# Optimization experiments

Hardware: AMD Instinct MI355X
Metric: run time of the kernel (lower is better)

The kernel has to match this reference:

```python
import jax, jax.numpy as jnp
import numpy as np

B, C, Np, D = 16, 64, 128, 128
HT = 4      # time heads
HS = 4      # space heads (GAT)
F = D       # GAT out_channels
DK = D // 2 # q/k proj dim
TOPK = 8
NEG = -1e30

def ln(x, g, b):
    m = x.mean(-1, keepdims=True)
    v = jnp.mean((x - m) ** 2, axis=-1, keepdims=True)
    return (x - m) / jnp.sqrt(v + 1e-5) * g + b

def setup_inputs() -> dict:
    key = jax.random.key(0)
    ks = jax.random.split(key, 16)
    w = lambda k, s: (jax.random.normal(k, s, jnp.float32) * 0.02)
    return dict(
        H_in=jax.random.normal(ks[0], (B, C, Np, D), jnp.float32),
        static_adj=jax.random.normal(ks[1], (C, C), jnp.float32) * 0.1,
        attn_in_w=w(ks[2], (3 * D, D)), attn_in_b=jnp.zeros((3 * D,), jnp.float32),
        attn_out_w=w(ks[3], (D, D)), attn_out_b=jnp.zeros((D,), jnp.float32),
        ln1_g=jnp.ones((D,), jnp.float32), ln1_b=jnp.zeros((D,), jnp.float32),
        ln2_g=jnp.ones((D,), jnp.float32), ln2_b=jnp.zeros((D,), jnp.float32),
        ff1_w=w(ks[4], (4 * D, D)), ff1_b=jnp.zeros((4 * D,), jnp.float32),
        ff2_w=w(ks[5], (D, 4 * D)), ff2_b=jnp.zeros((D,), jnp.float32),
        tnorm_g=jnp.ones((D,), jnp.float32), tnorm_b=jnp.zeros((D,), jnp.float32),
        q_w=w(ks[6], (DK, D)), q_b=jnp.zeros((DK,), jnp.float32),
        k_w=w(ks[7], (DK, D)), k_b=jnp.zeros((DK,), jnp.float32),
        gat_w=w(ks[8], (HS, F, D)),
        gat_att_src=w(ks[9], (HS, F)), gat_att_dst=w(ks[10], (HS, F)),
        gat_bias=jnp.zeros((D,), jnp.float32),
        snorm_g=jnp.ones((D,), jnp.float32), snorm_b=jnp.zeros((D,), jnp.float32),
    )

def _forward(H_in, static_adj, attn_in_w, attn_in_b, attn_out_w, attn_out_b,
             ln1_g, ln1_b, ln2_g, ln2_b, ff1_w, ff1_b, ff2_w, ff2_b,
             tnorm_g, tnorm_b, q_w, q_b, k_w, k_b,
             gat_w, gat_att_src, gat_att_dst, gat_bias, snorm_g, snorm_b):
    dh = D // HT
    # ---- temporal transformer encoder layer (norm_first) on [B*C, Np, D]
    x0 = H_in.reshape(B * C, Np, D)
    h = ln(x0, ln1_g, ln1_b)
    qkv = h @ attn_in_w.T + attn_in_b
    q, k, v = jnp.split(qkv, 3, axis=-1)
    q = q.reshape(-1, Np, HT, dh).transpose(0, 2, 1, 3)
    k = k.reshape(-1, Np, HT, dh).transpose(0, 2, 1, 3)
    v = v.reshape(-1, Np, HT, dh).transpose(0, 2, 1, 3)
    att = jax.nn.softmax(jnp.einsum('nhqd,nhkd->nhqk', q, k) / jnp.sqrt(jnp.float32(dh)), axis=-1)
    o = jnp.einsum('nhqk,nhkd->nhqd', att, v).transpose(0, 2, 1, 3).reshape(-1, Np, D)
    x = x0 + (o @ attn_out_w.T + attn_out_b)
    h2 = ln(x, ln2_g, ln2_b)
    x = x + jax.nn.relu(h2 @ ff1_w.T + ff1_b) @ ff2_w.T + ff2_b
    H_temp = ln(x0 + x, tnorm_g, tnorm_b).reshape(B, C, Np, D)
    # ---- dynamic adjacency from temporal summary
    Hs = H_temp.mean(axis=2)                              # [B,C,D]
    q2 = Hs @ q_w.T + q_b
    k2 = Hs @ k_w.T + k_b
    sim = jnp.einsum('bcd,bed->bce', q2, k2) * (DK ** -0.5)
    A = jnp.tanh(sim) + static_adj[None]                  # [B,C,C]
    # ---- top-k edge mask per sample (row r -> its top-k cols, no self loops)
    kk = max(1, min(TOPK, C - 1))
    idx = jax.lax.top_k(A, kk)[1]                         # [B,C,kk]
    mask = jnp.any(jax.nn.one_hot(idx, C, dtype=bool), axis=2)  # [B,C,C]
    mask = mask & (~jnp.eye(C, dtype=bool)) & (A != 0)
    # ---- dense masked GAT over all (B, Np) graphs; src=row, dst=col
    xh = jnp.einsum('bcpd,hfd->bphcf', H_temp, gat_w)     # [B,Np,HS,C,F]
    asrc = jnp.einsum('bphcf,hf->bphc', xh, gat_att_src)
    adst = jnp.einsum('bphcf,hf->bphc', xh, gat_att_dst)
    e = asrc[..., :, None] + adst[..., None, :]           # [B,Np,HS,src,dst]
    e = jnp.where(e > 0, e, 0.2 * e)                      # LeakyReLU(0.2)
    mb = mask[:, None, None, :, :]
    e = jnp.where(mb, e, NEG)
    e = e - e.max(axis=3, keepdims=True)                  # softmax over src per dst
    wgt = jnp.exp(e) * mb
    s = wgt.sum(axis=3, keepdims=True)
    a = wgt / jnp.where(s > 0, s, 1.0)
    out = jnp.einsum('bphst,bphsf->bphtf', a, xh).mean(axis=2) + gat_bias  # [B,Np,C,F]
    out = out.transpose(0, 2, 1, 3)                       # [B,C,Np,D]
    return ln(out + H_temp, snorm_g, snorm_b)

def reference(H_in, static_adj, attn_in_w, attn_in_b, attn_out_w, attn_out_b,
              ln1_g, ln1_b, ln2_g, ln2_b, ff1_w, ff1_b, ff2_w, ff2_b,
              tnorm_g, tnorm_b, q_w, q_b, k_w, k_b,
              gat_w, gat_att_src, gat_att_dst, gat_bias, snorm_g, snorm_b):
    return _forward(H_in, static_adj, attn_in_w, attn_in_b, attn_out_w, attn_out_b,
                    ln1_g, ln1_b, ln2_g, ln2_b, ff1_w, ff1_b, ff2_w, ff2_b,
                    tnorm_g, tnorm_b, q_w, q_b, k_w, k_b,
                    gat_w, gat_att_src, gat_att_dst, gat_bias, snorm_g, snorm_b)
```

## Files before the change

kernel.cpp:

```cpp
#include <hip/hip_runtime.h>
#include <cstdint>


typedef __attribute__((ext_vector_type(8)))  short bf16x8;
typedef __attribute__((ext_vector_type(16))) float f32x16;
#define MFMA32(a, b, c) __builtin_amdgcn_mfma_f32_32x32x16_bf16((a), (b), (c), 0, 0, 0)

__device__ __forceinline__ unsigned short f2bf(float f) {
    unsigned int u = __float_as_uint(f);
    u += 0x7fffu + ((u >> 16) & 1u);
    return (unsigned short)(u >> 16);
}
__device__ __forceinline__ float bf2f(unsigned short u) {
    return __uint_as_float(((unsigned int)u) << 16);
}

__device__ __forceinline__ bf16x8 lds_frag(const unsigned short* p) {
    union { bf16x8 v; ushort4 h[2]; } u;
    u.h[0] = *(const ushort4*)p;
    u.h[1] = *(const ushort4*)(p + 4);
    return u.v;
}
__device__ __forceinline__ bf16x8 gfrag(const unsigned short* p) {
    union { bf16x8 v; uint4 u; } t;
    t.u = *(const uint4*)p;
    return t.v;
}

__device__ __forceinline__ int rowmap(int r, int hl) { return (r & 3) + 8 * (r >> 2) + 4 * hl; }

__global__ void wconv_kernel(const float* __restrict__ wqkv, const float* __restrict__ wout,
                             const float* __restrict__ w1, const float* __restrict__ w2,
                             const float* __restrict__ gw,
                             unsigned short* __restrict__ dst) {
    int i = blockIdx.x * 256 + threadIdx.x;
    float v;
    if (i < 49152)       v = wqkv[i];
    else if (i < 65536)  v = wout[i - 49152];
    else if (i < 131072) v = w1[i - 65536];
    else if (i < 196608) v = w2[i - 131072];
    else                 v = gw[i - 196608];
    dst[i] = f2bf(v);
}

__global__ void wa_kernel(const float* __restrict__ gw, const float* __restrict__ asw,
                          const float* __restrict__ adw,
                          float* __restrict__ waS, float* __restrict__ waD) {
    int t = blockIdx.x * 256 + threadIdx.x;
    int h = t >> 8, d = (t >> 1) & 127, which = t & 1;
    const float* av = which ? adw : asw;
    float s = 0.f;
    for (int f = 0; f < 128; f++) s += av[h * 128 + f] * gw[(h * 128 + f) * 128 + d];
    (which ? waD : waS)[h * 128 + d] = s;
}

__global__ __launch_bounds__(256, 2)
void temporal_kernel(const float* __restrict__ Hin,
                     const unsigned short* __restrict__ wqkv_b, const float* __restrict__ bqkv,
                     const unsigned short* __restrict__ wout_b, const float* __restrict__ bout,
                     const float* __restrict__ g1, const float* __restrict__ b1,
                     const float* __restrict__ g2, const float* __restrict__ b2,
                     const unsigned short* __restrict__ w1_b, const float* __restrict__ bf1,
                     const unsigned short* __restrict__ w2_b, const float* __restrict__ bf2,
                     const float* __restrict__ tg, const float* __restrict__ tb,
                     float* __restrict__ Htemp) {
    __shared__ unsigned short RA[128][132];
    __shared__ double RBd[4512];
    unsigned short (*qb)[36]  = (unsigned short(*)[36])RBd;
    unsigned short (*kb)[36]  = (unsigned short(*)[36])((char*)RBd + 9216);
    unsigned short (*vT)[132] = (unsigned short(*)[132])((char*)RBd + 18432);
    unsigned short (*Pb)[36]  = (unsigned short(*)[36])((char*)RBd + 26880);
    unsigned short (*h2b)[132] = (unsigned short(*)[132])RBd;

    const int n = blockIdx.x;
    const int tid = threadIdx.x;
    const int lane = tid & 63;
    const int wv = tid >> 6;
    const int hl = lane >> 5;
    const int l31 = lane & 31;
    const int myrow = wv * 32 + l31;

    {
        int row = tid >> 1, hf = tid & 1;
        const float* src = Hin + ((long)n * 128 + row) * 128 + hf * 64;
        float xv[64];
        float s = 0.f, qs = 0.f;
#pragma unroll
        for (int i = 0; i < 64; i += 4) {
            float4 t = *(const float4*)(src + i);
            xv[i] = t.x; xv[i+1] = t.y; xv[i+2] = t.z; xv[i+3] = t.w;
        }
#pragma unroll
        for (int i = 0; i < 64; i++) { s += xv[i]; qs += xv[i] * xv[i]; }
        s += __shfl_xor(s, 1); qs += __shfl_xor(qs, 1);
        float mu = s * 0.0078125f;
        float rs = rsqrtf(fmaxf(qs * 0.0078125f - mu * mu, 0.f) + 1e-5f);
#pragma unroll
        for (int i = 0; i < 64; i++) {
            int d = hf * 64 + i;
            RA[row][d] = f2bf((xv[i] - mu) * rs * g1[d] + b1[d]);
        }
    }

    f32x16 oaccH[4];
#pragma unroll
    for (int h = 0; h < 4; h++)
#pragma unroll
        for (int r = 0; r < 16; r++) oaccH[h][r] = 0.f;

    for (int h = 0; h < 4; h++) {
        {
            f32x16 accq, acck, accv;
            float bq = bqkv[      h * 32 + l31];
            float bk = bqkv[128 + h * 32 + l31];
            float bv = bqkv[256 + h * 32 + l31];
#pragma unroll
            for (int r = 0; r < 16; r++) { accq[r] = bq; acck[r] = bk; accv[r] = bv; }
            const unsigned short* wq = wqkv_b + (      h * 32 + l31) * 128 + hl * 8;
            const unsigned short* wk = wqkv_b + (128 + h * 32 + l31) * 128 + hl * 8;
            const unsigned short* wvp= wqkv_b + (256 + h * 32 + l31) * 128 + hl * 8;
#pragma unroll
            for (int k0 = 0; k0 < 128; k0 += 16) {
                bf16x8 a  = lds_frag(&RA[myrow][k0 + hl * 8]);
                accq = MFMA32(a, gfrag(wq + k0), accq);
                acck = MFMA32(a, gfrag(wk + k0), acck);
                accv = MFMA32(a, gfrag(wvp + k0), accv);
            }
#pragma unroll
            for (int r = 0; r < 16; r++) {
                int tok = wv * 32 + rowmap(r, hl);
                qb[tok][l31] = f2bf(accq[r]);
                kb[tok][l31] = f2bf(acck[r]);
                vT[l31][tok] = f2bf(accv[r]);
            }
        }
        __syncthreads();

        f32x16 sacc[4];
#pragma unroll
        for (int t = 0; t < 4; t++)
#pragma unroll
            for (int r = 0; r < 16; r++) sacc[t][r] = 0.f;
#pragma unroll
        for (int k0 = 0; k0 < 32; k0 += 16) {
            bf16x8 a = lds_frag(&qb[myrow][k0 + hl * 8]);
#pragma unroll
            for (int t = 0; t < 4; t++) {
                bf16x8 b = lds_frag(&kb[t * 32 + l31][k0 + hl * 8]);
                sacc[t] = MFMA32(a, b, sacc[t]);
            }
        }
        const float scale = 0.17677669529663687f;
#pragma unroll
        for (int r = 0; r < 16; r++) {
            float m0 = fmaxf(fmaxf(sacc[0][r], sacc[1][r]), fmaxf(sacc[2][r], sacc[3][r]));
#pragma unroll
            for (int d = 1; d < 32; d <<= 1) m0 = fmaxf(m0, __shfl_xor(m0, d));
            float ssum = 0.f;
#pragma unroll
            for (int t = 0; t < 4; t++) {
                float e = __expf(scale * (sacc[t][r] - m0));
                sacc[t][r] = e; ssum += e;
            }
#pragma unroll
            for (int d = 1; d < 32; d <<= 1) ssum += __shfl_xor(ssum, d);
            float rinv = 1.f / ssum;
#pragma unroll
            for (int t = 0; t < 4; t++) sacc[t][r] *= rinv;
        }

#pragma unroll
        for (int t = 0; t < 4; t++) {
#pragma unroll
            for (int r = 0; r < 16; r++)
                Pb[wv * 32 + rowmap(r, hl)][l31] = f2bf(sacc[t][r]);
#pragma unroll
            for (int k0 = 0; k0 < 32; k0 += 16) {
                bf16x8 a = lds_frag(&Pb[wv * 32 + l31][k0 + hl * 8]);
                bf16x8 b = lds_frag(&vT[l31][t * 32 + k0 + hl * 8]);
                oaccH[h] = MFMA32(a, b, oaccH[h]);
            }
        }
        __syncthreads();
    }

#pragma unroll
    for (int h = 0; h < 4; h++)
#pragma unroll
        for (int r = 0; r < 16; r++) {
            int tok = wv * 32 + rowmap(r, hl);
            RA[tok][h * 32 + l31] = f2bf(oaccH[h][r]);
        }

    f32x16 acc[4];
#pragma unroll
    for (int t = 0; t < 4; t++) {
        float bo = bout[t * 32 + l31];
#pragma unroll
        for (int r = 0; r < 16; r++) {
            int tok = wv * 32 + rowmap(r, hl);
            acc[t][r] = Hin[((long)n * 128 + tok) * 128 + t * 32 + l31] + bo;
        }
    }
#pragma unroll
    for (int k0 = 0; k0 < 128; k0 += 16) {
        bf16x8 a = lds_frag(&RA[myrow][k0 + hl * 8]);
#pragma unroll
        for (int t = 0; t < 4; t++) {
            bf16x8 b = gfrag(wout_b + (t * 32 + l31) * 128 + k0 + hl * 8);
            acc[t] = MFMA32(a, b, acc[t]);
        }
    }

#pragma unroll
    for (int r = 0; r < 16; r++) {
        float s = acc[0][r] + acc[1][r] + acc[2][r] + acc[3][r];
#pragma unroll
        for (int d = 1; d < 32; d <<= 1) s += __shfl_xor(s, d);
        float mu = s * 0.0078125f;
        float q = 0.f;
#pragma unroll
        for (int t = 0; t < 4; t++) { float dv = acc[t][r] - mu; q += dv * dv; }
#pragma unroll
        for (int d = 1; d < 32; d <<= 1) q += __shfl_xor(q, d);
        float rs = rsqrtf(q * 0.0078125f + 1e-5f);
        int row = wv * 32 + rowmap(r, hl);
#pragma unroll
        for (int t = 0; t < 4; t++) {
            int col = t * 32 + l31;
            h2b[row][col] = f2bf((acc[t][r] - mu) * rs * g2[col] + b2[col]);
        }
    }

    f32x16 acc2[4];
#pragma unroll
    for (int t = 0; t < 4; t++) {
        float bv = bf2[t * 32 + l31];
#pragma unroll
        for (int r = 0; r < 16; r++) acc2[t][r] = acc[t][r] + bv;
    }

    for (int j = 0; j < 4; j++) {
        f32x16 racc[4];
#pragma unroll
        for (int t = 0; t < 4; t++) {
            float bv = bf1[j * 128 + t * 32 + l31];
#pragma unroll
            for (int r = 0; r < 16; r++) racc[t][r] = bv;
        }
#pragma unroll
        for (int k0 = 0; k0 < 128; k0 += 16) {
            bf16x8 a = lds_frag(&h2b[myrow][k0 + hl * 8]);
#pragma unroll
            for (int t = 0; t < 4; t++) {
                bf16x8 b = gfrag(w1_b + (j * 128 + t * 32 + l31) * 128 + k0 + hl * 8);
                racc[t] = MFMA32(a, b, racc[t]);
            }
        }
#pragma unroll
        for (int t = 0; t < 4; t++)
#pragma unroll
            for (int r = 0; r < 16; r++) {
                int row = wv * 32 + rowmap(r, hl);
                RA[row][t * 32 + l31] = f2bf(fmaxf(racc[t][r], 0.f));
            }
#pragma unroll
        for (int k0 = 0; k0 < 128; k0 += 16) {
            bf16x8 a = lds_frag(&RA[myrow][k0 + hl * 8]);
#pragma unroll
            for (int t = 0; t < 4; t++) {
                bf16x8 b = gfrag(w2_b + (t * 32 + l31) * 512 + j * 128 + k0 + hl * 8);
                acc2[t] = MFMA32(a, b, acc2[t]);
            }
        }
    }

#pragma unroll
    for (int t = 0; t < 4; t++)
#pragma unroll
        for (int r = 0; r < 16; r++) {
            int tok = wv * 32 + rowmap(r, hl);
            acc2[t][r] += Hin[((long)n * 128 + tok) * 128 + t * 32 + l31];
        }
    float* outf = Htemp + (long)n * 16384;
#pragma unroll
    for (int r = 0; r < 16; r++) {
        float s = acc2[0][r] + acc2[1][r] + acc2[2][r] + acc2[3][r];
#pragma unroll
        for (int d = 1; d < 32; d <<= 1) s += __shfl_xor(s, d);
        float mu = s * 0.0078125f;
        float q = 0.f;
#pragma unroll
        for (int t = 0; t < 4; t++) { float dv = acc2[t][r] - mu; q += dv * dv; }
#pragma unroll
        for (int d = 1; d < 32; d <<= 1) q += __shfl_xor(q, d);
        float rs = rsqrtf(q * 0.0078125f + 1e-5f);
        int tok = wv * 32 + rowmap(r, hl);
#pragma unroll
        for (int t = 0; t < 4; t++) {
            int col = t * 32 + l31;
            outf[tok * 128 + col] = (acc2[t][r] - mu) * rs * tg[col] + tb[col];
        }
    }
}

__global__ void hs_kernel(const float* __restrict__ Htemp, float* __restrict__ Hs) {
    int idx = blockIdx.x * 256 + threadIdx.x;
    int n = idx >> 7, d = idx & 127;
    float s = 0.f;
    for (int p = 0; p < 128; p++) s += Htemp[((long)n * 128 + p) * 128 + d];
    Hs[idx] = s * 0.0078125f;
}

__global__ __launch_bounds__(256)
void graph_kernel(const float* __restrict__ Hs,
                  const float* __restrict__ qw, const float* __restrict__ qb,
                  const float* __restrict__ kw, const float* __restrict__ kb,
                  const float* __restrict__ adj, unsigned long long* __restrict__ masks) {
    __shared__ float q2l[64][65];
    __shared__ float k2l[64][65];
    __shared__ float am[64][65];
    int b = blockIdx.x;
    int tid = threadIdx.x;
    {
        int r = tid & 127, jh = tid >> 7;
        int row = r & 63;
        const float* wmat = (r < 64) ? qw : kw;
        const float* bvec = (r < 64) ? qb : kb;
        const float* src = Hs + (long)(b * 64 + row) * 128;
        for (int jj = 0; jj < 32; jj++) {
            int j = jh * 32 + jj;
            const float* wrow = wmat + (long)j * 128;
            float s0 = 0.f, s1 = 0.f, s2 = 0.f, s3 = 0.f;
#pragma unroll
            for (int d = 0; d < 128; d += 4) {
                s0 += src[d] * wrow[d];     s1 += src[d+1] * wrow[d+1];
                s2 += src[d+2] * wrow[d+2]; s3 += src[d+3] * wrow[d+3];
            }
            float val = ((s0 + s1) + (s2 + s3)) + bvec[j];
            if (r < 64) q2l[row][j] = val; else k2l[row][j] = val;
        }
    }
    __syncthreads();
    {
        int c = tid & 63, eq = tid >> 6;
        for (int ee = 0; ee < 16; ee++) {
            int e = eq * 16 + ee;
            float s0 = 0.f, s1 = 0.f, s2 = 0.f, s3 = 0.f;
#pragma unroll
            for (int j = 0; j < 64; j += 4) {
                s0 += q2l[c][j]   * k2l[e][j];
                s1 += q2l[c][j+1] * k2l[e][j+1];
                s2 += q2l[c][j+2] * k2l[e][j+2];
                s3 += q2l[c][j+3] * k2l[e][j+3];
            }
            float sim = ((s0 + s1) + (s2 + s3)) * 0.125f;
            am[c][e] = tanhf(sim) + adj[c * 64 + e];
        }
    }
    __syncthreads();
    if (tid < 64) {
        int c = tid;
        unsigned long long sel = 0ull;
        for (int it = 0; it < 8; it++) {
            float best = -1e38f; int bi = 0;
            for (int e = 0; e < 64; e++) {
                float v = am[c][e];
                bool ok = (((sel >> e) & 1ull) == 0ull) && (v > best);
                best = ok ? v : best;
                bi = ok ? e : bi;
            }
            sel |= (1ull << bi);
        }
        sel &= ~(1ull << c);
        for (int e = 0; e < 64; e++)
            if (am[c][e] == 0.f) sel &= ~(1ull << e);
        masks[b * 64 + c] = sel;
    }
}

__global__ __launch_bounds__(256, 1)
void gat_kernel(float* __restrict__ Htemp,
                const unsigned short* __restrict__ gwb,
                const float* __restrict__ waS, const float* __restrict__ waD,
                const float* __restrict__ gbias,
                const unsigned long long* __restrict__ masks,
                const float* __restrict__ sg, const float* __restrict__ sb) {
    __shared__ unsigned short Htb[64][132];
    __shared__ double ovl_d[3264];
    __shared__ float asrcF[4][64], adstF[4][64];
    __shared__ float pmax[4][64], psum[4][64];
    __shared__ unsigned long long mk[64];

    unsigned short (*xhT)[68]  = (unsigned short(*)[68])ovl_d;
    unsigned short (*attT)[68] = (unsigned short(*)[68])((char*)ovl_d + 17408);
    float (*part)[8][64]       = (float(*)[8][64])ovl_d;

    const int bp = blockIdx.x;
    const int b = bp >> 7, p = bp & 127;
    const int tid = threadIdx.x;
    const int lane = tid & 63, wv = tid >> 6;
    const int hl = lane >> 5, l31 = lane & 31;
    const int rs = (wv & 1) * 32;
    const int cs = (wv >> 1) * 64;

    {
        int c = tid >> 2, qq = tid & 3;
        const float* src = Htemp + ((long)(b * 64 + c) * 128 + p) * 128 + qq * 32;
#pragma unroll
        for (int k = 0; k < 8; k++) {
            float4 t4 = *(const float4*)(src + 4 * k);
            ushort4 u; u.x = f2bf(t4.x); u.y = f2bf(t4.y); u.z = f2bf(t4.z); u.w = f2bf(t4.w);
            *(ushort4*)&Htb[c][qq * 32 + 4 * k] = u;
        }
    }
    if (tid < 64) mk[tid] = masks[b * 64 + tid];
    __syncthreads();

    {
        int s = lane, q = wv;
        float acc[8];
#pragma unroll
        for (int m = 0; m < 8; m++) acc[m] = 0.f;
        const unsigned int* hp = (const unsigned int*)&Htb[s][q * 32];
#pragma unroll
        for (int d2 = 0; d2 < 16; d2++) {
            unsigned int u = hp[d2];
            float f0 = __uint_as_float(u << 16);
            float f1 = __uint_as_float(u & 0xffff0000u);
            int d = q * 32 + 2 * d2;
#pragma unroll
            for (int h = 0; h < 4; h++) {
                acc[2*h]   += f0 * waS[h * 128 + d] + f1 * waS[h * 128 + d + 1];
                acc[2*h+1] += f0 * waD[h * 128 + d] + f1 * waD[h * 128 + d + 1];
            }
        }
#pragma unroll
        for (int m = 0; m < 8; m++) part[q][m][s] = acc[m];
    }
    __syncthreads();
    for (int o = tid; o < 512; o += 256) {
        int h = o >> 7, rem = o & 127, which = rem >> 6, s = rem & 63;
        int m = h * 2 + which;
        float v = part[0][m][s] + part[1][m][s] + part[2][m][s] + part[3][m][s];
        if (which == 0) asrcF[h][s] = v; else adstF[h][s] = v;
    }
    __syncthreads();

    f32x16 oacc0, oacc1;
#pragma unroll
    for (int r = 0; r < 16; r++) { oacc0[r] = 0.f; oacc1[r] = 0.f; }

    for (int h = 0; h < 4; h++) {
        f32x16 a0, a1;
#pragma unroll
        for (int r = 0; r < 16; r++) { a0[r] = 0.f; a1[r] = 0.f; }
        const unsigned short* gwh = gwb + h * 16384;
#pragma unroll
        for (int k0 = 0; k0 < 128; k0 += 16) {
            bf16x8 af = lds_frag(&Htb[rs + l31][k0 + hl * 8]);
            bf16x8 b0 = gfrag(gwh + (cs + l31) * 128 + k0 + hl * 8);
            bf16x8 b1 = gfrag(gwh + (cs + 32 + l31) * 128 + k0 + hl * 8);
            a0 = MFMA32(af, b0, a0);
            a1 = MFMA32(af, b1, a1);
        }
#pragma unroll
        for (int g = 0; g < 4; g++) {
            ushort4 u0, u1;
            u0.x = f2bf(a0[4*g]);   u0.y = f2bf(a0[4*g+1]);
            u0.z = f2bf(a0[4*g+2]); u0.w = f2bf(a0[4*g+3]);
            u1.x = f2bf(a1[4*g]);   u1.y = f2bf(a1[4*g+1]);
            u1.z = f2bf(a1[4*g+2]); u1.w = f2bf(a1[4*g+3]);
            int so = rs + 4 * hl + 8 * g;
            *(ushort4*)&xhT[cs + l31][so]      = u0;
            *(ushort4*)&xhT[cs + 32 + l31][so] = u1;
        }
        __syncthreads();

        {
            int t = lane;
            float adv = adstF[h][t];
            float ev[16];
            float mx = -1e30f;
#pragma unroll
            for (int i = 0; i < 16; i++) {
                int s = wv * 16 + i;
                float e = asrcF[h][s] + adv;
                e = (e > 0.f) ? e : 0.2f * e;
                ev[i] = e;
                if ((mk[s] >> t) & 1ull) mx = fmaxf(mx, e);
            }
            pmax[wv][t] = mx;
            __syncthreads();
            float M = fmaxf(fmaxf(pmax[0][t], pmax[1][t]), fmaxf(pmax[2][t], pmax[3][t]));
            float sm = 0.f;
#pragma unroll
            for (int i = 0; i < 16; i++) {
                int s = wv * 16 + i;
                float w = ((mk[s] >> t) & 1ull) ? __expf(ev[i] - M) : 0.f;
                ev[i] = w; sm += w;
            }
            psum[wv][t] = sm;
            __syncthreads();
            float S = psum[0][t] + psum[1][t] + psum[2][t] + psum[3][t];
            float rinv = (S > 0.f) ? 1.f / S : 0.f;
#pragma unroll
            for (int g = 0; g < 4; g++) {
                ushort4 u;
                u.x = f2bf(ev[4*g]   * rinv); u.y = f2bf(ev[4*g+1] * rinv);
                u.z = f2bf(ev[4*g+2] * rinv); u.w = f2bf(ev[4*g+3] * rinv);
                *(ushort4*)&attT[t][wv * 16 + 4 * g] = u;
            }
        }
        __syncthreads();

#pragma unroll
        for (int k0 = 0; k0 < 64; k0 += 16) {
            bf16x8 af = lds_frag(&attT[rs + l31][k0 + hl * 8]);
            bf16x8 b0 = lds_frag(&xhT[cs + l31][k0 + hl * 8]);
            bf16x8 b1 = lds_frag(&xhT[cs + 32 + l31][k0 + hl * 8]);
            oacc0 = MFMA32(af, b0, oacc0);
            oacc1 = MFMA32(af, b1, oacc1);
        }
        __syncthreads();
    }

    float gb0 = gbias[cs + l31], gb1 = gbias[cs + 32 + l31];
    float v0[16], v1[16];
#pragma unroll
    for (int r = 0; r < 16; r++) {
        int c = rs + rowmap(r, hl);
        v0[r] = oacc0[r] * 0.25f + gb0 + bf2f(Htb[c][cs + l31]);
        v1[r] = oacc1[r] * 0.25f + gb1 + bf2f(Htb[c][cs + 32 + l31]);
    }
#pragma unroll
    for (int r = 0; r < 16; r++) {
        float s = v0[r] + v1[r];
        float q = v0[r] * v0[r] + v1[r] * v1[r];
#pragma unroll
        for (int d = 1; d < 32; d <<= 1) { s += __shfl_xor(s, d); q += __shfl_xor(q, d); }
        if (l31 == 0) {
            int c = rs + rowmap(r, hl);
            pmax[wv >> 1][c] = s;
            psum[wv >> 1][c] = q;
        }
    }
    __syncthreads();
    float sgv0 = sg[cs + l31], sbv0 = sb[cs + l31];
    float sgv1 = sg[cs + 32 + l31], sbv1 = sb[cs + 32 + l31];
#pragma unroll
    for (int r = 0; r < 16; r++) {
        int c = rs + rowmap(r, hl);
        float sum = pmax[0][c] + pmax[1][c];
        float sq  = psum[0][c] + psum[1][c];
        float mu = sum * 0.0078125f;
        float var = sq * 0.0078125f - mu * mu;
        float rsd = rsqrtf(fmaxf(var, 0.f) + 1e-5f);
        float* orow = Htemp + ((long)(b * 64 + c) * 128 + p) * 128;
        orow[cs + l31]      = (v0[r] - mu) * rsd * sgv0 + sbv0;
        orow[cs + 32 + l31] = (v1[r] - mu) * rsd * sgv1 + sbv1;
    }
}

extern "C" void kernel_launch(void* const* d_in, const int* in_sizes, int n_in,
                              void* d_out, int out_size, void* d_ws, size_t ws_size,
                              hipStream_t stream) {
    const float* Hin        = (const float*)d_in[0];
    const float* static_adj = (const float*)d_in[1];
    const float* attn_in_w  = (const float*)d_in[2];
    const float* attn_in_b  = (const float*)d_in[3];
    const float* attn_out_w = (const float*)d_in[4];
    const float* attn_out_b = (const float*)d_in[5];
    const float* ln1_g      = (const float*)d_in[6];
    const float* ln1_b      = (const float*)d_in[7];
    const float* ln2_g      = (const float*)d_in[8];
    const float* ln2_b      = (const float*)d_in[9];
    const float* ff1_w      = (const float*)d_in[10];
    const float* ff1_b      = (const float*)d_in[11];
    const float* ff2_w      = (const float*)d_in[12];
    const float* ff2_b      = (const float*)d_in[13];
    const float* tnorm_g    = (const float*)d_in[14];
    const float* tnorm_b    = (const float*)d_in[15];
    const float* q_w        = (const float*)d_in[16];
    const float* q_b        = (const float*)d_in[17];
    const float* k_w        = (const float*)d_in[18];
    const float* k_b        = (const float*)d_in[19];
    const float* gat_w      = (const float*)d_in[20];
    const float* gat_att_src= (const float*)d_in[21];
    const float* gat_att_dst= (const float*)d_in[22];
    const float* gat_bias   = (const float*)d_in[23];
    const float* snorm_g    = (const float*)d_in[24];
    const float* snorm_b    = (const float*)d_in[25];

    float* out = (float*)d_out;
    char* ws = (char*)d_ws;
    unsigned short* wb = (unsigned short*)ws;
    const unsigned short* wqkv_b = wb;
    const unsigned short* wout_b = wb + 49152;
    const unsigned short* w1_b   = wb + 65536;
    const unsigned short* w2_b   = wb + 131072;
    const unsigned short* gw_b   = wb + 196608;
    unsigned long long* masks = (unsigned long long*)(ws + 524288);
    float* Hs  = (float*)(ws + 532480);
    float* waS = (float*)(ws + 1056768);
    float* waD = (float*)(ws + 1058816);

    hipLaunchKernelGGL(wconv_kernel, dim3(1024), dim3(256), 0, stream,
                       attn_in_w, attn_out_w, ff1_w, ff2_w, gat_w, wb);
    hipLaunchKernelGGL(wa_kernel, dim3(4), dim3(256), 0, stream,
                       gat_w, gat_att_src, gat_att_dst, waS, waD);
    hipLaunchKernelGGL(temporal_kernel, dim3(1024), dim3(256), 0, stream,
                       Hin, wqkv_b, attn_in_b, wout_b, attn_out_b,
                       ln1_g, ln1_b, ln2_g, ln2_b,
                       w1_b, ff1_b, w2_b, ff2_b, tnorm_g, tnorm_b, out);
    hipLaunchKernelGGL(hs_kernel, dim3(512), dim3(256), 0, stream, out, Hs);
    hipLaunchKernelGGL(graph_kernel, dim3(16), dim3(256), 0, stream,
                       Hs, q_w, q_b, k_w, k_b, static_adj, masks);
    hipLaunchKernelGGL(gat_kernel, dim3(2048), dim3(256), 0, stream,
                       out, gw_b, waS, waD, gat_bias,
                       masks, snorm_g, snorm_b);
}
```

Measured before the change: 621.9 us.

## Keep Q and P in registers via permlane swaps and shrink LDS for occupancy

The temporal kernel now computes Q transposed (weights as the A operand) and packs the accumulator directly into MFMA B-fragments with v_permlane32_swap. This drops the qb LDS buffer. The softmax probabilities are repacked the same way instead of going through the Pb LDS buffer, and with the transposed layout the row reductions need only one cross-lane shuffle instead of five. The FFN hidden activations go through a small per-wave scratch and layernorm output reuses RA, so LDS shrinks and launch bounds rise to 3 blocks per CU. The risk is register pressure at the higher occupancy target, which could cause spills.

```diff
diff --git a/kernel.cpp b/kernel.cpp
--- a/kernel.cpp
+++ b/kernel.cpp
@@ -28,6 +28,23 @@
 }
 
 __device__ __forceinline__ int rowmap(int r, int hl) { return (r & 3) + 8 * (r >> 2) + 4 * hl; }
+
+__device__ __forceinline__ unsigned int pk2(float lo, float hi) {
+    return (unsigned int)f2bf(lo) | ((unsigned int)f2bf(hi) << 16);
+}
+
+template<int B>
+__device__ __forceinline__ bf16x8 pack_frag(const f32x16& p) {
+    unsigned int a0 = pk2(p[B + 0], p[B + 1]);
+    unsigned int a1 = pk2(p[B + 2], p[B + 3]);
+    unsigned int b0 = pk2(p[B + 4], p[B + 5]);
+    unsigned int b1 = pk2(p[B + 6], p[B + 7]);
+    asm("v_permlane32_swap_b32 %0, %1" : "+v"(b0), "+v"(a0));
+    asm("v_permlane32_swap_b32 %0, %1" : "+v"(b1), "+v"(a1));
+    union { bf16x8 v; unsigned int w[4]; } u;
+    u.w[0] = a0; u.w[1] = a1; u.w[2] = b0; u.w[3] = b1;
+    return u.v;
+}
 
 __global__ void wconv_kernel(const float* __restrict__ wqkv, const float* __restrict__ wout,
                              const float* __restrict__ w1, const float* __restrict__ w2,
@@ -54,7 +71,7 @@
     (which ? waD : waS)[h * 128 + d] = s;
 }
 
-__global__ __launch_bounds__(256, 2)
+__global__ __launch_bounds__(256, 3)
 void temporal_kernel(const float* __restrict__ Hin,
                      const unsigned short* __restrict__ wqkv_b, const float* __restrict__ bqkv,
                      const unsigned short* __restrict__ wout_b, const float* __restrict__ bout,
@@ -65,12 +82,10 @@
                      const float* __restrict__ tg, const float* __restrict__ tb,
                      float* __restrict__ Htemp) {
     __shared__ unsigned short RA[128][132];
-    __shared__ double RBd[4512];
-    unsigned short (*qb)[36]  = (unsigned short(*)[36])RBd;
-    unsigned short (*kb)[36]  = (unsigned short(*)[36])((char*)RBd + 9216);
-    unsigned short (*vT)[132] = (unsigned short(*)[132])((char*)RBd + 18432);
-    unsigned short (*Pb)[36]  = (unsigned short(*)[36])((char*)RBd + 26880);
-    unsigned short (*h2b)[132] = (unsigned short(*)[132])RBd;
+    __shared__ double RBd[2208];
+    unsigned short (*kb)[36]  = (unsigned short(*)[36])RBd;
+    unsigned short (*vT)[132] = (unsigned short(*)[132])((char*)RBd + 9216);
+    unsigned short (*rscr)[32][36] = (unsigned short(*)[32][36])RBd;
 
     const int n = blockIdx.x;
     const int tid = threadIdx.x;
@@ -109,30 +124,33 @@
         for (int r = 0; r < 16; r++) oaccH[h][r] = 0.f;
 
     for (int h = 0; h < 4; h++) {
+        bf16x8 qf0, qf1;
         {
             f32x16 accq, acck, accv;
-            float bq = bqkv[      h * 32 + l31];
+#pragma unroll
+            for (int r = 0; r < 16; r++) accq[r] = bqkv[h * 32 + rowmap(r, hl)];
             float bk = bqkv[128 + h * 32 + l31];
             float bv = bqkv[256 + h * 32 + l31];
 #pragma unroll
-            for (int r = 0; r < 16; r++) { accq[r] = bq; acck[r] = bk; accv[r] = bv; }
+            for (int r = 0; r < 16; r++) { acck[r] = bk; accv[r] = bv; }
             const unsigned short* wq = wqkv_b + (      h * 32 + l31) * 128 + hl * 8;
             const unsigned short* wk = wqkv_b + (128 + h * 32 + l31) * 128 + hl * 8;
             const unsigned short* wvp= wqkv_b + (256 + h * 32 + l31) * 128 + hl * 8;
 #pragma unroll
             for (int k0 = 0; k0 < 128; k0 += 16) {
                 bf16x8 a  = lds_frag(&RA[myrow][k0 + hl * 8]);
-                accq = MFMA32(a, gfrag(wq + k0), accq);
+                accq = MFMA32(gfrag(wq + k0), a, accq);
                 acck = MFMA32(a, gfrag(wk + k0), acck);
                 accv = MFMA32(a, gfrag(wvp + k0), accv);
             }
 #pragma unroll
             for (int r = 0; r < 16; r++) {
                 int tok = wv * 32 + rowmap(r, hl);
-                qb[tok][l31] = f2bf(accq[r]);
                 kb[tok][l31] = f2bf(acck[r]);
                 vT[l31][tok] = f2bf(accv[r]);
             }
+            qf0 = pack_frag<0>(accq);
+            qf1 = pack_frag<8>(accq);
         }
         __syncthreads();
 
@@ -142,44 +160,42 @@
 #pragma unroll
             for (int r = 0; r < 16; r++) sacc[t][r] = 0.f;
 #pragma unroll
-        for (int k0 = 0; k0 < 32; k0 += 16) {
-            bf16x8 a = lds_frag(&qb[myrow][k0 + hl * 8]);
-#pragma unroll
-            for (int t = 0; t < 4; t++) {
-                bf16x8 b = lds_frag(&kb[t * 32 + l31][k0 + hl * 8]);
-                sacc[t] = MFMA32(a, b, sacc[t]);
-            }
+        for (int t = 0; t < 4; t++) {
+            bf16x8 ka0 = lds_frag(&kb[t * 32 + l31][hl * 8]);
+            sacc[t] = MFMA32(ka0, qf0, sacc[t]);
+            bf16x8 ka1 = lds_frag(&kb[t * 32 + l31][16 + hl * 8]);
+            sacc[t] = MFMA32(ka1, qf1, sacc[t]);
         }
         const float scale = 0.17677669529663687f;
-#pragma unroll
-        for (int r = 0; r < 16; r++) {
-            float m0 = fmaxf(fmaxf(sacc[0][r], sacc[1][r]), fmaxf(sacc[2][r], sacc[3][r]));
-#pragma unroll
-            for (int d = 1; d < 32; d <<= 1) m0 = fmaxf(m0, __shfl_xor(m0, d));
-            float ssum = 0.f;
-#pragma unroll
-            for (int t = 0; t < 4; t++) {
+        float m0 = -1e30f;
+#pragma unroll
+        for (int t = 0; t < 4; t++)
+#pragma unroll
+            for (int r = 0; r < 16; r++) m0 = fmaxf(m0, sacc[t][r]);
+        m0 = fmaxf(m0, __shfl_xor(m0, 32));
+        float ssum = 0.f;
+#pragma unroll
+        for (int t = 0; t < 4; t++)
+#pragma unroll
+            for (int r = 0; r < 16; r++) {
                 float e = __expf(scale * (sacc[t][r] - m0));
                 sacc[t][r] = e; ssum += e;
             }
-#pragma unroll
-            for (int d = 1; d < 32; d <<= 1) ssum += __shfl_xor(ssum, d);
-            float rinv = 1.f / ssum;
-#pragma unroll
-            for (int t = 0; t < 4; t++) sacc[t][r] *= rinv;
-        }
+        ssum += __shfl_xor(ssum, 32);
+        float rinv = 1.f / ssum;
+#pragma unroll
+        for (int t = 0; t < 4; t++)
+#pragma unroll
+            for (int r = 0; r < 16; r++) sacc[t][r] *= rinv;
 
 #pragma unroll
         for (int t = 0; t < 4; t++) {
-#pragma unroll
-            for (int r = 0; r < 16; r++)
-                Pb[wv * 32 + rowmap(r, hl)][l31] = f2bf(sacc[t][r]);
-#pragma unroll
-            for (int k0 = 0; k0 < 32; k0 += 16) {
-                bf16x8 a = lds_frag(&Pb[wv * 32 + l31][k0 + hl * 8]);
-                bf16x8 b = lds_frag(&vT[l31][t * 32 + k0 + hl * 8]);
-                oaccH[h] = MFMA32(a, b, oaccH[h]);
-            }
+            bf16x8 pf0 = pack_frag<0>(sacc[t]);
+            bf16x8 v0  = lds_frag(&vT[l31][t * 32 + hl * 8]);
+            oaccH[h] = MFMA32(pf0, v0, oaccH[h]);
+            bf16x8 pf1 = pack_frag<8>(sacc[t]);
+            bf16x8 v1  = lds_frag(&vT[l31][t * 32 + 16 + hl * 8]);
+            oaccH[h] = MFMA32(pf1, v1, oaccH[h]);
         }
         __syncthreads();
     }
@@ -228,7 +244,7 @@
 #pragma unroll
         for (int t = 0; t < 4; t++) {
             int col = t * 32 + l31;
-            h2b[row][col] = f2bf((acc[t][r] - mu) * rs * g2[col] + b2[col]);
+            RA[row][col] = f2bf((acc[t][r] - mu) * rs * g2[col] + b2[col]);
         }
     }
 
@@ -250,7 +266,7 @@
         }
 #pragma unroll
         for (int k0 = 0; k0 < 128; k0 += 16) {
-            bf16x8 a = lds_frag(&h2b[myrow][k0 + hl * 8]);
+            bf16x8 a = lds_frag(&RA[myrow][k0 + hl * 8]);
 #pragma unroll
             for (int t = 0; t < 4; t++) {
                 bf16x8 b = gfrag(w1_b + (j * 128 + t * 32 + l31) * 128 + k0 + hl * 8);
@@ -258,19 +274,18 @@
             }
         }
 #pragma unroll
-        for (int t = 0; t < 4; t++)
-#pragma unroll
-            for (int r = 0; r < 16; r++) {
-                int row = wv * 32 + rowmap(r, hl);
-                RA[row][t * 32 + l31] = f2bf(fmaxf(racc[t][r], 0.f));
-            }
-#pragma unroll
-        for (int k0 = 0; k0 < 128; k0 += 16) {
-            bf16x8 a = lds_frag(&RA[myrow][k0 + hl * 8]);
-#pragma unroll
-            for (int t = 0; t < 4; t++) {
-                bf16x8 b = gfrag(w2_b + (t * 32 + l31) * 512 + j * 128 + k0 + hl * 8);
-                acc2[t] = MFMA32(a, b, acc2[t]);
+        for (int t = 0; t < 4; t++) {
+#pragma unroll
+            for (int r = 0; r < 16; r++)
+                rscr[wv][rowmap(r, hl)][l31] = f2bf(fmaxf(racc[t][r], 0.f));
+#pragma unroll
+            for (int kk = 0; kk < 32; kk += 16) {
+                bf16x8 a = lds_frag(&rscr[wv][l31][kk + hl * 8]);
+#pragma unroll
+                for (int tp = 0; tp < 4; tp++) {
+                    bf16x8 b = gfrag(w2_b + (tp * 32 + l31) * 512 + j * 128 + t * 32 + kk + hl * 8);
+                    acc2[tp] = MFMA32(a, b, acc2[tp]);
+                }
             }
         }
     }
```

Measured after the change: 693.7 us. +11.6%, slower.
